# Performance work log

Measured on AMD Instinct MI355X. Metric: run time of the kernel, lower is better.

Reference implementation:

```python
import jax, jax.numpy as jnp
import numpy as np
from jax import lax

WIN = 9            # NCC_vxm default local window per dim
ITER_COUNT = 5
REG_WEIGHT = 1.0
LR, B1, B2, EPS = 0.1, 0.9, 0.999, 1e-8  # Adam(amsgrad=True) defaults + lr=0.1


def _window_sum(t, win=WIN):
    """Sum over a win^3 neighborhood (= conv3d with ones kernel, pad win//2),
    computed separably along each spatial axis. t: [B,1,H,W,D]."""
    pad = win // 2
    for ax in range(3):
        kshape = [1, 1, 1, 1, 1]
        kshape[2 + ax] = win
        k = jnp.ones(kshape, t.dtype)
        padding = [(pad, pad) if j == ax else (0, 0) for j in range(3)]
        t = lax.conv_general_dilated(t, k, (1, 1, 1), padding,
                                     dimension_numbers=('NCDHW', 'OIDHW', 'NCDHW'))
    return t


def ncc_loss(I, J):
    """voxelmorph local NCC (NCC_vxm), returns -mean(cc)."""
    win_size = float(WIN ** 3)
    I_sum = _window_sum(I)
    J_sum = _window_sum(J)
    I2_sum = _window_sum(I * I)
    J2_sum = _window_sum(J * J)
    IJ_sum = _window_sum(I * J)
    u_I = I_sum / win_size
    u_J = J_sum / win_size
    cross = IJ_sum - u_J * I_sum - u_I * J_sum + u_I * u_J * win_size
    I_var = I2_sum - 2.0 * u_I * I_sum + u_I * u_I * win_size
    J_var = J2_sum - 2.0 * u_J * J_sum + u_J * u_J * win_size
    cc = cross * cross / (I_var * J_var + 1e-5)
    return -jnp.mean(cc)


def grad3d_l2(flow):
    """Grad3d(penalty='l2'): mean squared finite differences, averaged over 3 axes."""
    dH = jnp.mean((flow[:, :, 1:] - flow[:, :, :-1]) ** 2)
    dW = jnp.mean((flow[:, :, :, 1:] - flow[:, :, :, :-1]) ** 2)
    dD = jnp.mean((flow[:, :, :, :, 1:] - flow[:, :, :, :, :-1]) ** 2)
    return (dH + dW + dD) / 3.0


def warp(x, flow):
    """SpatialTransformer: trilinear resample of x at (identity grid + flow),
    zero padding outside (torch grid_sample align_corners=True, padding 'zeros').
    x: [B,C,H,W,D], flow: [B,3,H,W,D]."""
    B, C, H, W, D = x.shape
    base = jnp.stack(jnp.meshgrid(jnp.arange(H, dtype=x.dtype),
                                  jnp.arange(W, dtype=x.dtype),
                                  jnp.arange(D, dtype=x.dtype),
                                  indexing='ij'), axis=0)          # [3,H,W,D]
    coords = base[None] + flow                                      # [B,3,H,W,D]

    def samp_one(vol, crd):  # vol [H,W,D], crd [3,H,W,D]
        return jax.scipy.ndimage.map_coordinates(
            vol, [crd[0], crd[1], crd[2]], order=1, mode='constant', cval=0.0)

    samp_batch = jax.vmap(lambda v, c: jax.vmap(lambda ch: samp_one(ch, c))(v))
    return samp_batch(x, coords)                                    # [B,C,H,W,D]


def _optimize_flow(x, y, initial_flow):
    """Inner OFG loop: 5 Adam(amsgrad) steps on the flow parameter."""
    def inner_loss(flow):
        x_warped = warp(x, flow)
        return ncc_loss(x_warped, y) + REG_WEIGHT * grad3d_l2(flow)

    grad_fn = jax.grad(inner_loss)
    flow = initial_flow
    m = jnp.zeros_like(flow)
    v = jnp.zeros_like(flow)
    vhat = jnp.zeros_like(flow)
    for t in range(1, ITER_COUNT + 1):
        g = grad_fn(flow)
        m = B1 * m + (1.0 - B1) * g
        v = B2 * v + (1.0 - B2) * g * g
        vhat = jnp.maximum(vhat, v)           # amsgrad
        m_hat = m / (1.0 - B1 ** t)
        denom = jnp.sqrt(vhat) / jnp.sqrt(1.0 - B2 ** t) + EPS
        flow = flow - LR * m_hat / denom
    return flow


def setup_inputs() -> dict:
    key = jax.random.key(0)
    k1, k2, k3 = jax.random.split(key, 3)
    H, W, D = 160, 192, 160
    x = jax.random.normal(k1, (1, 1, H, W, D), dtype=jnp.float32)
    y = jax.random.normal(k2, (1, 1, H, W, D), dtype=jnp.float32)
    initial_flow = jax.random.normal(k3, (1, 3, H, W, D), dtype=jnp.float32)
    return {"x": x, "y": y, "initial_flow": initial_flow}


def reference(x, y, initial_flow):
    flow = _optimize_flow(x, y, initial_flow)
    return jnp.mean((flow - initial_flow) ** 2)   # nn.MSELoss()
```

## Files before the change

kernel.cpp:

```cpp
#include <hip/hip_runtime.h>
#include <cmath>

#define HH 160
#define WW 192
#define DD 160
#define WD (WW*DD)
#define NPTS (HH*WW*DD)
#define NP4  (NPTS/4)
#define INV_WSZ (1.0f/729.0f)
#define ADAM_B1 0.9f
#define ADAM_B2 0.999f
#define ADAM_LR 0.1f
#define ADAM_EPS 1e-8f
#define NBLK_FINAL 4800

__device__ __align__(16) float g_flowA[3*NPTS];
__device__ __align__(16) float g_flowB[3*NPTS];
__device__ __align__(16) float g_m   [3*NPTS];
__device__ __align__(16) float g_v   [3*NPTS];
__device__ __align__(16) float g_vh  [3*NPTS];
__device__ __align__(16) float g_X   [3*NPTS];
__device__ __align__(16) float g_Y   [3*NPTS];
__device__ __align__(16) float g_I   [NPTS];
__device__ __align__(16) float g_G   [3*NPTS];
__device__ __align__(16) float g_uJ  [NPTS];
__device__ __align__(16) float g_Jv  [NPTS];
__device__ double g_part[8192];


typedef float nat4 __attribute__((ext_vector_type(4)));

__device__ __forceinline__ float4 ld4(const float* p) { return *reinterpret_cast<const float4*>(p); }
__device__ __forceinline__ void  st4(float* p, float4 v) { *reinterpret_cast<float4*>(p) = v; }
__device__ __forceinline__ float4 ld4nt(const float* p) {
    nat4 t = __builtin_nontemporal_load(reinterpret_cast<const nat4*>(p));
    return float4{t.x, t.y, t.z, t.w};
}
__device__ __forceinline__ void st4nt(float* p, float4 v) {
    nat4 t = {v.x, v.y, v.z, v.w};
    __builtin_nontemporal_store(t, reinterpret_cast<nat4*>(p));
}
#define UNPK(V,A) { A[0]=(V).x; A[1]=(V).y; A[2]=(V).z; A[3]=(V).w; }

__device__ __forceinline__ float fetchx(const float* __restrict__ x, int i, int j, int k) {
    if ((unsigned)i >= (unsigned)HH || (unsigned)j >= (unsigned)WW || (unsigned)k >= (unsigned)DD)
        return 0.0f;
    return x[(i*WW + j)*DD + k];
}

__device__ __forceinline__ void load12(const float* base, int idx, int dp, float* t) {
    float4 a = (dp == 0)    ? float4{0,0,0,0} : ld4(base + idx - 4);
    float4 b = ld4(base + idx);
    float4 c = (dp == DD-4) ? float4{0,0,0,0} : ld4(base + idx + 4);
    t[0]=a.x; t[1]=a.y; t[2]=a.z; t[3]=a.w;
    t[4]=b.x; t[5]=b.y; t[6]=b.z; t[7]=b.w;
    t[8]=c.x; t[9]=c.y; t[10]=c.z; t[11]=c.w;
}

__global__ void __launch_bounds__(320) warp_momD_k(
        const float* __restrict__ x, const float* __restrict__ y,
        const float* __restrict__ finit, int fin_code)
{
    __shared__ __align__(16) float sI[8][168];
    __shared__ __align__(16) float sJ[8][168];
    int tx = threadIdx.x;
    int ty = threadIdx.y;
    int line = blockIdx.x*8 + ty;
    int h = line / WW, w = line % WW;
    int dp = tx*4;
    int idx = line*DD + dp;
    const float* fin = (fin_code == 0) ? finit : ((fin_code == 1) ? g_flowA : g_flowB);

    float F0[4], F1[4], F2[4], Y4[4];
    { float4 a = ld4(fin + idx);          UNPK(a, F0); }
    { float4 a = ld4(fin + NPTS + idx);   UNPK(a, F1); }
    { float4 a = ld4(fin + 2*NPTS + idx); UNPK(a, F2); }
    { float4 a = ld4(y + idx);            UNPK(a, Y4); }

    float GX[4], GY[4], GZ[4], IV[4];
#pragma unroll
    for (int e = 0; e < 4; e++) {
        float c0 = (float)h + F0[e];
        float c1 = (float)w + F1[e];
        float c2 = (float)(dp + e) + F2[e];
        float fl0 = floorf(c0), fl1 = floorf(c1), fl2 = floorf(c2);
        int i0 = (int)fl0, j0 = (int)fl1, k0 = (int)fl2;
        float fx = c0 - fl0, fy = c1 - fl1, fz = c2 - fl2;
        float v000 = fetchx(x, i0,   j0,   k0  ), v001 = fetchx(x, i0,   j0,   k0+1);
        float v010 = fetchx(x, i0,   j0+1, k0  ), v011 = fetchx(x, i0,   j0+1, k0+1);
        float v100 = fetchx(x, i0+1, j0,   k0  ), v101 = fetchx(x, i0+1, j0,   k0+1);
        float v110 = fetchx(x, i0+1, j0+1, k0  ), v111 = fetchx(x, i0+1, j0+1, k0+1);
        float c00 = v000*(1.0f-fz) + v001*fz;
        float c01 = v010*(1.0f-fz) + v011*fz;
        float c10 = v100*(1.0f-fz) + v101*fz;
        float c11 = v110*(1.0f-fz) + v111*fz;
        float a0 = c00*(1.0f-fy) + c01*fy;
        float a1 = c10*(1.0f-fy) + c11*fy;
        float Ival = a0*(1.0f-fx) + a1*fx;
        IV[e] = Ival;
        sI[ty][4+dp+e] = Ival;
        sJ[ty][4+dp+e] = Y4[e];
        GX[e] = (1.0f-fy)*((v100-v000)*(1.0f-fz) + (v101-v001)*fz)
              +        fy*((v110-v010)*(1.0f-fz) + (v111-v011)*fz);
        GY[e] = (1.0f-fx)*((v010-v000)*(1.0f-fz) + (v011-v001)*fz)
              +        fx*((v110-v100)*(1.0f-fz) + (v111-v101)*fz);
        GZ[e] = (1.0f-fx)*((v001-v000)*(1.0f-fy) + (v011-v010)*fy)
              +        fx*((v101-v100)*(1.0f-fy) + (v111-v110)*fy);
    }
    st4nt(g_I + idx,          float4{IV[0],IV[1],IV[2],IV[3]});
    st4nt(g_G + idx,          float4{GX[0],GX[1],GX[2],GX[3]});
    st4nt(g_G + NPTS + idx,   float4{GY[0],GY[1],GY[2],GY[3]});
    st4nt(g_G + 2*NPTS + idx, float4{GZ[0],GZ[1],GZ[2],GZ[3]});

    if (tx == 0) {
#pragma unroll
        for (int j = 0; j < 4; j++) { sI[ty][j] = 0.f; sJ[ty][j] = 0.f; }
    }
    if (tx == 39) {
#pragma unroll
        for (int j = 164; j < 168; j++) { sI[ty][j] = 0.f; sJ[ty][j] = 0.f; }
    }
    __syncthreads();

    float tI[12], tJ[12];
    { float4 a = ld4(&sI[ty][dp]);   UNPK(a, (&tI[0])); }
    { float4 a = ld4(&sI[ty][dp+4]); UNPK(a, (&tI[4])); }
    { float4 a = ld4(&sI[ty][dp+8]); UNPK(a, (&tI[8])); }
    { float4 a = ld4(&sJ[ty][dp]);   UNPK(a, (&tJ[0])); }
    { float4 a = ld4(&sJ[ty][dp+4]); UNPK(a, (&tJ[4])); }
    { float4 a = ld4(&sJ[ty][dp+8]); UNPK(a, (&tJ[8])); }

    float s1a[4], s2a[4], s3a[4];
#pragma unroll
    for (int e = 0; e < 4; e++) {
        float s1 = 0.f, s2 = 0.f, s3 = 0.f;
#pragma unroll
        for (int j = 0; j < 9; j++) {
            float a = tI[e+j], b = tJ[e+j];
            s1 += a; s2 += a*a; s3 += a*b;
        }
        s1a[e] = s1; s2a[e] = s2; s3a[e] = s3;
    }
    st4nt(g_X + idx,          float4{s1a[0],s1a[1],s1a[2],s1a[3]});
    st4nt(g_X + NPTS + idx,   float4{s2a[0],s2a[1],s2a[2],s2a[3]});
    st4nt(g_X + 2*NPTS + idx, float4{s3a[0],s3a[1],s3a[2],s3a[3]});
}

template<int NF>
__global__ void __launch_bounds__(256) boxW_k()
{
    __shared__ __align__(16) float s[WW][32];
    int h  = blockIdx.x;
    int d0 = blockIdx.y*32;
    int t  = threadIdx.x;
#pragma unroll
    for (int f = 0; f < NF; f++) {
        const float* base = g_X + f*NPTS + h*WD + d0;
        for (int q = t; q < WW*8; q += 256) {
            int wq = q >> 3, dq = (q & 7)*4;
            st4(&s[wq][dq], ld4nt(base + wq*DD + dq));
        }
        __syncthreads();
        float* ob = g_Y + f*NPTS + h*WD + d0;
        for (int q = t; q < WW*8; q += 256) {
            int wq = q >> 3, dq = (q & 7)*4;
            int lo = (wq < 4) ? -wq : -4;
            int hi = (wq > WW-5) ? (WW-1-wq) : 4;
            float4 acc = float4{0,0,0,0};
            for (int k = lo; k <= hi; k++) {
                float4 v = ld4(&s[wq+k][dq]);
                acc.x += v.x; acc.y += v.y; acc.z += v.z; acc.w += v.w;
            }
            st4nt(ob + wq*DD + dq, acc);
        }
        __syncthreads();
    }
}

__global__ void __launch_bounds__(256) boxH_fields_k()
{
    __shared__ __align__(16) float sf[3][HH][16];
    int w  = blockIdx.x;
    int d0 = blockIdx.y*16;
    int t  = threadIdx.x;

#pragma unroll
    for (int f = 0; f < 3; f++) {
        const float* base = g_Y + f*NPTS + w*DD + d0;
        for (int q = t; q < HH*4; q += 256) {
            int hh = q >> 2, dq = (q & 3)*4;
            int lo = (hh < 4) ? -hh : -4;
            int hi = (hh > HH-5) ? (HH-1-hh) : 4;
            float4 acc = float4{0,0,0,0};
            for (int k = lo; k <= hi; k++) {
                float4 v = ld4(base + (hh+k)*WD + dq);
                acc.x += v.x; acc.y += v.y; acc.z += v.z; acc.w += v.w;
            }
            st4(&sf[f][hh][dq], acc);
        }
    }
    __syncthreads();

    {
        float A_[2][4], B_[2][4], C_[2][4];
        int qi = 0;
        for (int q = t; q < HH*4; q += 256, qi++) {
            int hh = q >> 2, dq = (q & 3)*4;
            int idxg = hh*WD + w*DD + d0 + dq;
            float Is[4], I2s[4], IJs[4], UJ[4], JV[4];
            { float4 a = ld4(&sf[0][hh][dq]); UNPK(a, Is); }
            { float4 a = ld4(&sf[1][hh][dq]); UNPK(a, I2s); }
            { float4 a = ld4(&sf[2][hh][dq]); UNPK(a, IJs); }
            { float4 a = ld4(g_uJ + idxg);    UNPK(a, UJ); }
            { float4 a = ld4(g_Jv + idxg);    UNPK(a, JV); }
#pragma unroll
            for (int e = 0; e < 4; e++) {
                float uI = Is[e] * INV_WSZ;
                float cross = IJs[e] - UJ[e]*Is[e];
                float Ivar  = I2s[e] - uI*Is[e];
                float den = Ivar*JV[e] + 1e-5f;
                float inv = 1.0f / den;
                float A = 2.0f*cross*inv;
                float B = -cross*cross*JV[e]*inv*inv;
                A_[qi][e] = A; B_[qi][e] = B; C_[qi][e] = A*UJ[e] + 2.0f*B*uI;
            }
        }
        __syncthreads();
        qi = 0;
        for (int q = t; q < HH*4; q += 256, qi++) {
            int hh = q >> 2, dq = (q & 3)*4;
            st4(&sf[0][hh][dq], float4{A_[qi][0],A_[qi][1],A_[qi][2],A_[qi][3]});
            st4(&sf[1][hh][dq], float4{B_[qi][0],B_[qi][1],B_[qi][2],B_[qi][3]});
            st4(&sf[2][hh][dq], float4{C_[qi][0],C_[qi][1],C_[qi][2],C_[qi][3]});
        }
    }
    __syncthreads();

#pragma unroll
    for (int f = 0; f < 3; f++) {
        float* ob = g_X + f*NPTS + w*DD + d0;
        for (int q = t; q < HH*4; q += 256) {
            int hh = q >> 2, dq = (q & 3)*4;
            int lo = (hh < 4) ? -hh : -4;
            int hi = (hh > HH-5) ? (HH-1-hh) : 4;
            float4 acc = float4{0,0,0,0};
            for (int k = lo; k <= hi; k++) {
                float4 v = ld4(&sf[f][hh+k][dq]);
                acc.x += v.x; acc.y += v.y; acc.z += v.z; acc.w += v.w;
            }
            st4nt(ob + hh*WD + dq, acc);
        }
    }
}

template<bool FINAL>
__global__ void __launch_bounds__(256) grad_adam_k(
        const float* __restrict__ y,
        const float* __restrict__ finit,
        int fin_code, int fout_code,
        float inv_bc1, float inv_sqrt_bc2, int is_first)
{
    __shared__ double sd[256];
    int p = blockIdx.x*blockDim.x + threadIdx.x;
    if (p >= NP4) return;
    int line = p / (DD/4);
    int dp   = (p % (DD/4))*4;
    int idx  = line*DD + dp;
    int w = line % WW;
    int h = line / WW;
    const float* fin = (fin_code == 0) ? finit : ((fin_code == 1) ? g_flowA : g_flowB);
    float* fout = (fout_code == 1) ? g_flowA : g_flowB;

    float SA[4], SB[4], SC[4];
    {
        float t[12];
        load12(g_Y,          idx, dp, t);
#pragma unroll
        for (int e = 0; e < 4; e++) { float s=0.f;
#pragma unroll
            for (int j = 0; j < 9; j++) s += t[e+j]; SA[e]=s; }
        load12(g_Y + NPTS,   idx, dp, t);
#pragma unroll
        for (int e = 0; e < 4; e++) { float s=0.f;
#pragma unroll
            for (int j = 0; j < 9; j++) s += t[e+j]; SB[e]=s; }
        load12(g_Y + 2*NPTS, idx, dp, t);
#pragma unroll
        for (int e = 0; e < 4; e++) { float s=0.f;
#pragma unroll
            for (int j = 0; j < 9; j++) s += t[e+j]; SC[e]=s; }
    }

    float F[3][4];
    { float4 a = ld4(fin + idx);          UNPK(a, F[0]); }
    { float4 a = ld4(fin + NPTS + idx);   UNPK(a, F[1]); }
    { float4 a = ld4(fin + 2*NPTS + idx); UNPK(a, F[2]); }
    float Y4[4], I4[4], GX[4], GY[4], GZ[4];
    { float4 a = ld4(y + idx);              UNPK(a, Y4); }
    { float4 a = ld4nt(g_I + idx);          UNPK(a, I4); }
    { float4 a = ld4nt(g_G + idx);          UNPK(a, GX); }
    { float4 a = ld4nt(g_G + NPTS + idx);   UNPK(a, GY); }
    { float4 a = ld4nt(g_G + 2*NPTS + idx); UNPK(a, GZ); }

    float GS[3][4];
#pragma unroll
    for (int e = 0; e < 4; e++) {
        float gI = -(1.0f/(float)NPTS) * (Y4[e]*SA[e] + 2.0f*I4[e]*SB[e] - SC[e]);
        GS[0][e] = gI*GX[e]; GS[1][e] = gI*GY[e]; GS[2][e] = gI*GZ[e];
    }

    const float coefH = 2.0f / (3.0f * (float)(3*(HH-1)*WW*DD));
    const float coefW = 2.0f / (3.0f * (float)(3*HH*(WW-1)*DD));
    const float coefD = 2.0f / (3.0f * (float)(3*HH*WW*(DD-1)));

    double msea = 0.0;

#pragma unroll
    for (int c = 0; c < 3; c++) {
        const float* fc = fin + c*NPTS;
        int o = c*NPTS + idx;
        float FU[4], FD[4], FL[4], FR[4];
        { float4 a = (h > 0)    ? ld4(fc + idx - WD) : float4{0,0,0,0}; UNPK(a, FU); }
        { float4 a = (h < HH-1) ? ld4(fc + idx + WD) : float4{0,0,0,0}; UNPK(a, FD); }
        { float4 a = (w > 0)    ? ld4(fc + idx - DD) : float4{0,0,0,0}; UNPK(a, FL); }
        { float4 a = (w < WW-1) ? ld4(fc + idx + DD) : float4{0,0,0,0}; UNPK(a, FR); }
        float dl = (dp > 0)     ? fc[idx - 1] : 0.f;
        float dr = (dp < DD-4)  ? fc[idx + 4] : 0.f;

        float M[4], V[4], VH[4];
        if (is_first) {
#pragma unroll
            for (int e = 0; e < 4; e++) { M[e]=0.f; V[e]=0.f; VH[e]=0.f; }
        } else {
            { float4 a = ld4nt(g_m  + o); UNPK(a, M); }
            { float4 a = ld4nt(g_v  + o); UNPK(a, V); }
            { float4 a = ld4nt(g_vh + o); UNPK(a, VH); }
        }

        float FI[4];
        if (FINAL) { float4 a = ld4(finit + o); UNPK(a, FI); }

        float O[4];
#pragma unroll
        for (int e = 0; e < 4; e++) {
            int d = dp + e;
            float f0 = F[c][e];
            float r = 0.0f;
            if (h > 0)     r += coefH*(f0 - FU[e]);
            if (h < HH-1)  r -= coefH*(FD[e] - f0);
            if (w > 0)     r += coefW*(f0 - FL[e]);
            if (w < WW-1)  r -= coefW*(FR[e] - f0);
            float left  = (e == 0) ? dl : F[c][e-1];
            float right = (e == 3) ? dr : F[c][e+1];
            if (d > 0)     r += coefD*(f0 - left);
            if (d < DD-1)  r -= coefD*(right - f0);
            float g = GS[c][e] + r;

            float mm  = ADAM_B1*M[e]  + (1.0f - ADAM_B1)*g;
            float vv  = ADAM_B2*V[e]  + (1.0f - ADAM_B2)*g*g;
            float vhh = fmaxf(VH[e], vv);
            M[e] = mm; V[e] = vv; VH[e] = vhh;
            float den = sqrtf(vhh)*inv_sqrt_bc2 + ADAM_EPS;
            O[e] = f0 - ADAM_LR*(mm*inv_bc1)/den;
            if (FINAL) {
                float df = O[e] - FI[e];
                msea += (double)df * (double)df;
            }
        }
        if (!FINAL) {
            st4nt(g_m  + o, float4{M[0],M[1],M[2],M[3]});
            st4nt(g_v  + o, float4{V[0],V[1],V[2],V[3]});
            st4nt(g_vh + o, float4{VH[0],VH[1],VH[2],VH[3]});
            st4(fout + o, float4{O[0],O[1],O[2],O[3]});
        }
    }

    if (FINAL) {
        int tid = threadIdx.x;
        sd[tid] = msea; __syncthreads();
        for (int o2 = 128; o2 > 0; o2 >>= 1) {
            if (tid < o2) sd[tid] += sd[tid + o2];
            __syncthreads();
        }
        if (tid == 0) g_part[blockIdx.x] = sd[0];
    }
}


__global__ void jmomD_k(const float* __restrict__ J)
{
    __shared__ float sJ[2][DD];
    int tx = threadIdx.x, ty = threadIdx.y;
    int line = blockIdx.x*2 + ty;
    int idx = line*DD + tx;
    sJ[ty][tx] = J[idx];
    __syncthreads();
    int lo = (tx < 4) ? -tx : -4;
    int hi = (tx > DD-5) ? (DD-1-tx) : 4;
    float s1 = 0.f, s2 = 0.f;
    for (int k = lo; k <= hi; k++) {
        float b = sJ[ty][tx+k];
        s1 += b; s2 += b*b;
    }
    g_X[idx] = s1; g_X[NPTS + idx] = s2;
}

__global__ void __launch_bounds__(256) boxH2_jstats_k()
{
    int p = blockIdx.x*blockDim.x + threadIdx.x;
    if (p >= NP4) return;
    int idx = p*4;
    int h = idx / WD;
    int lo = (h < 4) ? -h : -4;
    int hi = (h > HH-5) ? (HH-1-h) : 4;
    float4 s1 = float4{0,0,0,0}, s2 = float4{0,0,0,0};
    for (int k = lo; k <= hi; k++) {
        float4 a = ld4(g_Y + idx + k*WD);
        float4 b = ld4(g_Y + NPTS + idx + k*WD);
        s1.x += a.x; s1.y += a.y; s1.z += a.z; s1.w += a.w;
        s2.x += b.x; s2.y += b.y; s2.z += b.z; s2.w += b.w;
    }
    float4 u  = float4{s1.x*INV_WSZ, s1.y*INV_WSZ, s1.z*INV_WSZ, s1.w*INV_WSZ};
    float4 jv = float4{s2.x - u.x*s1.x, s2.y - u.y*s1.y, s2.z - u.z*s1.z, s2.w - u.w*s1.w};
    st4(g_uJ + idx, u);
    st4(g_Jv + idx, jv);
}


__global__ void mse_final_k(int nblk, float* __restrict__ out)
{
    __shared__ double sd[256];
    int tid = threadIdx.x;
    double s = 0.0;
    for (int i = tid; i < nblk; i += 256) s += g_part[i];
    sd[tid] = s; __syncthreads();
    for (int o = 128; o > 0; o >>= 1) {
        if (tid < o) sd[tid] += sd[tid + o];
        __syncthreads();
    }
    if (tid == 0) out[0] = (float)(sd[0] / (3.0*(double)NPTS));
}


extern "C" void kernel_launch(void* const* d_in, const int* in_sizes, int n_in,
                              void* d_out, int out_size, void* d_ws, size_t ws_size,
                              hipStream_t stream)
{
    const float* x    = (const float*)d_in[0];
    const float* y    = (const float*)d_in[1];
    const float* finit= (const float*)d_in[2];
    (void)d_ws; (void)ws_size;

    dim3 blk(256);
    dim3 grd4((NP4 + 255)/256);
    dim3 lineBlk(DD, 2);
    dim3 lineGrd(HH*WW/2);
    dim3 wBlk(256);
    dim3 wGrd(HH, DD/32);
    dim3 hGrd(WW, DD/16);
    dim3 wmBlk(40, 8);
    dim3 wmGrd(HH*WW/8);

    jmomD_k<<<lineGrd, lineBlk, 0, stream>>>(y);
    boxW_k<2><<<wGrd, wBlk, 0, stream>>>();
    boxH2_jstats_k<<<grd4, blk, 0, stream>>>();

    int fin_code = 0, fout_code = 1;
    for (int t = 1; t <= 5; t++) {
        warp_momD_k<<<wmGrd, wmBlk, 0, stream>>>(x, y, finit, fin_code);
        boxW_k<3><<<wGrd, wBlk, 0, stream>>>();
        boxH_fields_k<<<hGrd, blk, 0, stream>>>();
        boxW_k<3><<<wGrd, wBlk, 0, stream>>>();
        double bc1 = 1.0 - pow(0.9, (double)t);
        double bc2 = 1.0 - pow(0.999, (double)t);
        if (t < 5) {
            grad_adam_k<false><<<grd4, blk, 0, stream>>>(y, finit, fin_code, fout_code,
                                                         (float)(1.0/bc1), (float)(1.0/sqrt(bc2)),
                                                         (t == 1) ? 1 : 0);
        } else {
            grad_adam_k<true><<<grd4, blk, 0, stream>>>(y, finit, fin_code, fout_code,
                                                        (float)(1.0/bc1), (float)(1.0/sqrt(bc2)), 0);
        }
        fin_code = fout_code;
        fout_code = (fout_code == 1) ? 2 : 1;
    }

    mse_final_k<<<1, blk, 0, stream>>>(NBLK_FINAL, (float*)d_out);
}
```

Baseline: 1.799 ms.

## Stage box-filter inputs in LDS and split W-box fields across grid z

The W-direction box filter now gives each field its own block along grid z instead of looping over fields inside one block, which raises parallelism and removes per-field barriers. The H-direction pass of boxH_fields_k first stages each field column into zero-padded shared memory and sums nine rows from LDS, rather than issuing nine strided global loads per output. grad_adam_k is remapped to 40x8 line blocks that stage the three Y fields in padded shared rows for the D-direction window sums, and its final reduction is rewritten for 320 threads. This adds shared-memory traffic and extra barriers in exchange for fewer redundant global reads and more blocks in flight.

```diff
diff --git a/kernel.cpp b/kernel.cpp
--- a/kernel.cpp
+++ b/kernel.cpp
@@ -12,7 +12,7 @@
 #define ADAM_B2 0.999f
 #define ADAM_LR 0.1f
 #define ADAM_EPS 1e-8f
-#define NBLK_FINAL 4800
+#define NBLK_FINAL 3840
 
 __device__ __align__(16) float g_flowA[3*NPTS];
 __device__ __align__(16) float g_flowB[3*NPTS];
@@ -46,15 +46,6 @@
     if ((unsigned)i >= (unsigned)HH || (unsigned)j >= (unsigned)WW || (unsigned)k >= (unsigned)DD)
         return 0.0f;
     return x[(i*WW + j)*DD + k];
-}
-
-__device__ __forceinline__ void load12(const float* base, int idx, int dp, float* t) {
-    float4 a = (dp == 0)    ? float4{0,0,0,0} : ld4(base + idx - 4);
-    float4 b = ld4(base + idx);
-    float4 c = (dp == DD-4) ? float4{0,0,0,0} : ld4(base + idx + 4);
-    t[0]=a.x; t[1]=a.y; t[2]=a.z; t[3]=a.w;
-    t[4]=b.x; t[5]=b.y; t[6]=b.z; t[7]=b.w;
-    t[8]=c.x; t[9]=c.y; t[10]=c.z; t[11]=c.w;
 }
 
 __global__ void __launch_bounds__(320) warp_momD_k(
@@ -146,73 +137,81 @@
     st4nt(g_X + 2*NPTS + idx, float4{s3a[0],s3a[1],s3a[2],s3a[3]});
 }
 
-template<int NF>
-__global__ void __launch_bounds__(256) boxW_k()
+__global__ void __launch_bounds__(256) boxW1_k()
 {
     __shared__ __align__(16) float s[WW][32];
     int h  = blockIdx.x;
     int d0 = blockIdx.y*32;
+    int f  = blockIdx.z;
     int t  = threadIdx.x;
-#pragma unroll
-    for (int f = 0; f < NF; f++) {
-        const float* base = g_X + f*NPTS + h*WD + d0;
-        for (int q = t; q < WW*8; q += 256) {
-            int wq = q >> 3, dq = (q & 7)*4;
-            st4(&s[wq][dq], ld4nt(base + wq*DD + dq));
-        }
-        __syncthreads();
-        float* ob = g_Y + f*NPTS + h*WD + d0;
-        for (int q = t; q < WW*8; q += 256) {
-            int wq = q >> 3, dq = (q & 7)*4;
-            int lo = (wq < 4) ? -wq : -4;
-            int hi = (wq > WW-5) ? (WW-1-wq) : 4;
-            float4 acc = float4{0,0,0,0};
-            for (int k = lo; k <= hi; k++) {
-                float4 v = ld4(&s[wq+k][dq]);
-                acc.x += v.x; acc.y += v.y; acc.z += v.z; acc.w += v.w;
-            }
-            st4nt(ob + wq*DD + dq, acc);
-        }
-        __syncthreads();
+    const float* base = g_X + f*NPTS + h*WD + d0;
+    for (int q = t; q < WW*8; q += 256) {
+        int wq = q >> 3, dq = (q & 7)*4;
+        st4(&s[wq][dq], ld4nt(base + wq*DD + dq));
+    }
+    __syncthreads();
+    float* ob = g_Y + f*NPTS + h*WD + d0;
+    for (int q = t; q < WW*8; q += 256) {
+        int wq = q >> 3, dq = (q & 7)*4;
+        int lo = (wq < 4) ? -wq : -4;
+        int hi = (wq > WW-5) ? (WW-1-wq) : 4;
+        float4 acc = float4{0,0,0,0};
+        for (int k = lo; k <= hi; k++) {
+            float4 v = ld4(&s[wq+k][dq]);
+            acc.x += v.x; acc.y += v.y; acc.z += v.z; acc.w += v.w;
+        }
+        st4nt(ob + wq*DD + dq, acc);
     }
 }
 
 __global__ void __launch_bounds__(256) boxH_fields_k()
 {
-    __shared__ __align__(16) float sf[3][HH][16];
+    __shared__ __align__(16) float sa[(HH+8)*16];
+    __shared__ __align__(16) float sf[3][HH*16];
     int w  = blockIdx.x;
     int d0 = blockIdx.y*16;
     int t  = threadIdx.x;
 
+    if (t < 32) {
+        int r = t >> 2, cq = (t & 3)*4;
+        int row = (r < 4) ? r : (HH + r);
+        st4(&sa[row*16 + cq], float4{0,0,0,0});
+    }
+
 #pragma unroll
     for (int f = 0; f < 3; f++) {
         const float* base = g_Y + f*NPTS + w*DD + d0;
+        __syncthreads();
         for (int q = t; q < HH*4; q += 256) {
             int hh = q >> 2, dq = (q & 3)*4;
-            int lo = (hh < 4) ? -hh : -4;
-            int hi = (hh > HH-5) ? (HH-1-hh) : 4;
+            st4(&sa[(hh+4)*16 + dq], ld4nt(base + hh*WD + dq));
+        }
+        __syncthreads();
+        for (int q = t; q < HH*4; q += 256) {
+            int hh = q >> 2, dq = (q & 3)*4;
             float4 acc = float4{0,0,0,0};
-            for (int k = lo; k <= hi; k++) {
-                float4 v = ld4(base + (hh+k)*WD + dq);
+#pragma unroll
+            for (int k = 0; k < 9; k++) {
+                float4 v = ld4(&sa[(hh+k)*16 + dq]);
                 acc.x += v.x; acc.y += v.y; acc.z += v.z; acc.w += v.w;
             }
-            st4(&sf[f][hh][dq], acc);
+            st4(&sf[f][hh*16 + dq], acc);
         }
     }
     __syncthreads();
 
     {
-        float A_[2][4], B_[2][4], C_[2][4];
+        float A_[3][4], B_[3][4], C_[3][4];
         int qi = 0;
         for (int q = t; q < HH*4; q += 256, qi++) {
             int hh = q >> 2, dq = (q & 3)*4;
             int idxg = hh*WD + w*DD + d0 + dq;
             float Is[4], I2s[4], IJs[4], UJ[4], JV[4];
-            { float4 a = ld4(&sf[0][hh][dq]); UNPK(a, Is); }
-            { float4 a = ld4(&sf[1][hh][dq]); UNPK(a, I2s); }
-            { float4 a = ld4(&sf[2][hh][dq]); UNPK(a, IJs); }
-            { float4 a = ld4(g_uJ + idxg);    UNPK(a, UJ); }
-            { float4 a = ld4(g_Jv + idxg);    UNPK(a, JV); }
+            { float4 a = ld4(&sf[0][hh*16 + dq]); UNPK(a, Is); }
+            { float4 a = ld4(&sf[1][hh*16 + dq]); UNPK(a, I2s); }
+            { float4 a = ld4(&sf[2][hh*16 + dq]); UNPK(a, IJs); }
+            { float4 a = ld4(g_uJ + idxg);        UNPK(a, UJ); }
+            { float4 a = ld4(g_Jv + idxg);        UNPK(a, JV); }
 #pragma unroll
             for (int e = 0; e < 4; e++) {
                 float uI = Is[e] * INV_WSZ;
@@ -229,9 +228,9 @@
         qi = 0;
         for (int q = t; q < HH*4; q += 256, qi++) {
             int hh = q >> 2, dq = (q & 3)*4;
-            st4(&sf[0][hh][dq], float4{A_[qi][0],A_[qi][1],A_[qi][2],A_[qi][3]});
-            st4(&sf[1][hh][dq], float4{B_[qi][0],B_[qi][1],B_[qi][2],B_[qi][3]});
-            st4(&sf[2][hh][dq], float4{C_[qi][0],C_[qi][1],C_[qi][2],C_[qi][3]});
+            st4(&sf[0][hh*16 + dq], float4{A_[qi][0],A_[qi][1],A_[qi][2],A_[qi][3]});
+            st4(&sf[1][hh*16 + dq], float4{B_[qi][0],B_[qi][1],B_[qi][2],B_[qi][3]});
+            st4(&sf[2][hh*16 + dq], float4{C_[qi][0],C_[qi][1],C_[qi][2],C_[qi][3]});
         }
     }
     __syncthreads();
@@ -245,7 +244,7 @@
             int hi = (hh > HH-5) ? (HH-1-hh) : 4;
             float4 acc = float4{0,0,0,0};
             for (int k = lo; k <= hi; k++) {
-                float4 v = ld4(&sf[f][hh+k][dq]);
+                float4 v = ld4(&sf[f][(hh+k)*16 + dq]);
                 acc.x += v.x; acc.y += v.y; acc.z += v.z; acc.w += v.w;
             }
             st4nt(ob + hh*WD + dq, acc);
@@ -254,41 +253,60 @@
 }
 
 template<bool FINAL>
-__global__ void __launch_bounds__(256) grad_adam_k(
+__global__ void __launch_bounds__(320) grad_adam_k(
         const float* __restrict__ y,
         const float* __restrict__ finit,
         int fin_code, int fout_code,
         float inv_bc1, float inv_sqrt_bc2, int is_first)
 {
-    __shared__ double sd[256];
-    int p = blockIdx.x*blockDim.x + threadIdx.x;
-    if (p >= NP4) return;
-    int line = p / (DD/4);
-    int dp   = (p % (DD/4))*4;
-    int idx  = line*DD + dp;
-    int w = line % WW;
-    int h = line / WW;
+    __shared__ __align__(16) float sY[3][8][168];
+    __shared__ double sd[FINAL ? 320 : 1];
+    int tx = threadIdx.x;
+    int ty = threadIdx.y;
+    int line = blockIdx.x*8 + ty;
+    int h = line / WW, w = line % WW;
+    int dp = tx*4;
+    int idx = line*DD + dp;
     const float* fin = (fin_code == 0) ? finit : ((fin_code == 1) ? g_flowA : g_flowB);
     float* fout = (fout_code == 1) ? g_flowA : g_flowB;
 
+#pragma unroll
+    for (int f = 0; f < 3; f++)
+        st4(&sY[f][ty][4+dp], ld4nt(g_Y + f*NPTS + idx));
+    if (tx == 0) {
+#pragma unroll
+        for (int f = 0; f < 3; f++) st4(&sY[f][ty][0], float4{0,0,0,0});
+    }
+    if (tx == 39) {
+#pragma unroll
+        for (int f = 0; f < 3; f++) st4(&sY[f][ty][164], float4{0,0,0,0});
+    }
+    __syncthreads();
+
     float SA[4], SB[4], SC[4];
     {
-        float t[12];
-        load12(g_Y,          idx, dp, t);
+        float tW[12];
+        { float4 a = ld4(&sY[0][ty][dp]);   UNPK(a, (&tW[0])); }
+        { float4 a = ld4(&sY[0][ty][dp+4]); UNPK(a, (&tW[4])); }
+        { float4 a = ld4(&sY[0][ty][dp+8]); UNPK(a, (&tW[8])); }
 #pragma unroll
         for (int e = 0; e < 4; e++) { float s=0.f;
 #pragma unroll
-            for (int j = 0; j < 9; j++) s += t[e+j]; SA[e]=s; }
-        load12(g_Y + NPTS,   idx, dp, t);
+            for (int j = 0; j < 9; j++) s += tW[e+j]; SA[e]=s; }
+        { float4 a = ld4(&sY[1][ty][dp]);   UNPK(a, (&tW[0])); }
+        { float4 a = ld4(&sY[1][ty][dp+4]); UNPK(a, (&tW[4])); }
+        { float4 a = ld4(&sY[1][ty][dp+8]); UNPK(a, (&tW[8])); }
 #pragma unroll
         for (int e = 0; e < 4; e++) { float s=0.f;
 #pragma unroll
-            for (int j = 0; j < 9; j++) s += t[e+j]; SB[e]=s; }
-        load12(g_Y + 2*NPTS, idx, dp, t);
+            for (int j = 0; j < 9; j++) s += tW[e+j]; SB[e]=s; }
+        { float4 a = ld4(&sY[2][ty][dp]);   UNPK(a, (&tW[0])); }
+        { float4 a = ld4(&sY[2][ty][dp+4]); UNPK(a, (&tW[4])); }
+        { float4 a = ld4(&sY[2][ty][dp+8]); UNPK(a, (&tW[8])); }
 #pragma unroll
         for (int e = 0; e < 4; e++) { float s=0.f;
 #pragma unroll
-            for (int j = 0; j < 9; j++) s += t[e+j]; SC[e]=s; }
+            for (int j = 0; j < 9; j++) s += tW[e+j]; SC[e]=s; }
     }
 
     float F[3][4];
@@ -376,13 +394,15 @@
     }
 
     if (FINAL) {
-        int tid = threadIdx.x;
+        int tid = ty*40 + tx;
         sd[tid] = msea; __syncthreads();
-        for (int o2 = 128; o2 > 0; o2 >>= 1) {
-            if (tid < o2) sd[tid] += sd[tid + o2];
-            __syncthreads();
-        }
-        if (tid == 0) g_part[blockIdx.x] = sd[0];
+        if (tid < 160) sd[tid] += sd[tid + 160]; __syncthreads();
+        if (tid < 80)  sd[tid] += sd[tid + 80];  __syncthreads();
+        if (tid < 40)  sd[tid] += sd[tid + 40];  __syncthreads();
+        if (tid < 20)  sd[tid] += sd[tid + 20];  __syncthreads();
+        if (tid < 10)  sd[tid] += sd[tid + 10];  __syncthreads();
+        if (tid < 5)   sd[tid] += sd[tid + 5];   __syncthreads();
+        if (tid == 0) g_part[blockIdx.x] = sd[0] + sd[1] + sd[2] + sd[3] + sd[4];
     }
 }
 
@@ -455,31 +475,31 @@
     dim3 grd4((NP4 + 255)/256);
     dim3 lineBlk(DD, 2);
     dim3 lineGrd(HH*WW/2);
-    dim3 wBlk(256);
-    dim3 wGrd(HH, DD/32);
+    dim3 wGrd2(HH, DD/32, 2);
+    dim3 wGrd3(HH, DD/32, 3);
     dim3 hGrd(WW, DD/16);
     dim3 wmBlk(40, 8);
     dim3 wmGrd(HH*WW/8);
 
     jmomD_k<<<lineGrd, lineBlk, 0, stream>>>(y);
-    boxW_k<2><<<wGrd, wBlk, 0, stream>>>();
+    boxW1_k<<<wGrd2, blk, 0, stream>>>();
     boxH2_jstats_k<<<grd4, blk, 0, stream>>>();
 
     int fin_code = 0, fout_code = 1;
     for (int t = 1; t <= 5; t++) {
         warp_momD_k<<<wmGrd, wmBlk, 0, stream>>>(x, y, finit, fin_code);
-        boxW_k<3><<<wGrd, wBlk, 0, stream>>>();
+        boxW1_k<<<wGrd3, blk, 0, stream>>>();
         boxH_fields_k<<<hGrd, blk, 0, stream>>>();
-        boxW_k<3><<<wGrd, wBlk, 0, stream>>>();
+        boxW1_k<<<wGrd3, blk, 0, stream>>>();
         double bc1 = 1.0 - pow(0.9, (double)t);
         double bc2 = 1.0 - pow(0.999, (double)t);
         if (t < 5) {
-            grad_adam_k<false><<<grd4, blk, 0, stream>>>(y, finit, fin_code, fout_code,
-                                                         (float)(1.0/bc1), (float)(1.0/sqrt(bc2)),
-                                                         (t == 1) ? 1 : 0);
+            grad_adam_k<false><<<wmGrd, wmBlk, 0, stream>>>(y, finit, fin_code, fout_code,
+                                                            (float)(1.0/bc1), (float)(1.0/sqrt(bc2)),
+                                                            (t == 1) ? 1 : 0);
         } else {
-            grad_adam_k<true><<<grd4, blk, 0, stream>>>(y, finit, fin_code, fout_code,
-                                                        (float)(1.0/bc1), (float)(1.0/sqrt(bc2)), 0);
+            grad_adam_k<true><<<wmGrd, wmBlk, 0, stream>>>(y, finit, fin_code, fout_code,
+                                                           (float)(1.0/bc1), (float)(1.0/sqrt(bc2)), 0);
         }
         fin_code = fout_code;
         fout_code = (fout_code == 1) ? 2 : 1;
```

New measurement: 2.088 ms. +16.0%, slower.
